# Kernel optimization log

Measured on AMD Instinct MI355X. Metric: run time of the kernel, lower is better.

Reference implementation:

```python
import jax, jax.numpy as jnp
import numpy as np

T, B, M = 2048, 256, 32


def setup_inputs() -> dict:
    key = jax.random.key(0)
    k1, k2, k3, k4 = jax.random.split(key, 4)
    emissions = jax.random.normal(k1, (T, B, M), jnp.float32)
    tags = jax.random.randint(k2, (T, B), 0, M)
    # weight divides transition scores -> keep strictly positive
    weight = jax.random.uniform(k3, (T, B), jnp.float32, 0.5, 1.5)
    mask = jnp.ones((T, B), jnp.int32)  # first timestep must be all-on
    transitions = jax.random.normal(k4, (M, M), jnp.float32) * 0.1
    start_transitions = jnp.zeros((M,), jnp.float32)
    end_transitions = jnp.zeros((M,), jnp.float32)
    return {
        "emissions": emissions,
        "tags": tags,
        "weight": weight,
        "mask": mask,
        "transitions": transitions,
        "start_transitions": start_transitions,
        "end_transitions": end_transitions,
    }


def reference(emissions, tags, weight, mask, transitions, start_transitions, end_transitions):
    # emissions: [T,B,M]; tags/weight/mask: [T,B]; reduction='sum' (torch default)
    Tn, Bn, Mn = emissions.shape
    maskb = mask.astype(bool)
    tags = jnp.where(maskb, tags, 1)
    maskf = mask.astype(emissions.dtype)

    # ---- gold-path score (_compute_score) ----
    score = start_transitions[tags[0]]
    score = score + (transitions[tags[:-1], tags[1:]] * maskf[1:] / weight[:-1]).sum(0)
    em_sc = jnp.take_along_axis(emissions, tags[:, :, None], axis=-1)[..., 0] * maskf
    score = score + em_sc.sum(0)
    seq_ends = mask.astype(jnp.int32).sum(0) - 1  # [B]
    last_tags = tags[seq_ends, jnp.arange(Bn)]
    score = score + end_transitions[last_tags]

    # ---- log-partition (_compute_normalizer) via logsumexp-semiring scan ----
    neg_inf = jnp.asarray(-jnp.inf, emissions.dtype)
    log_eye = jnp.where(jnp.eye(Mn, dtype=bool), jnp.zeros((), emissions.dtype), neg_inf)

    alpha0 = start_transitions + emissions[0]  # [B,M]

    def step(alpha, xs):
        em_t, w_t, m_t = xs  # [B,M], [B], [B]
        sc = transitions[None, :, :] / w_t[:, None, None] + em_t[:, None, :]  # [B,M,M]
        sc = jnp.where(m_t[:, None, None], sc, log_eye)  # masked step = identity in log-semiring
        alpha = jax.nn.logsumexp(alpha[:, :, None] + sc, axis=1)
        return alpha, None

    alpha, _ = jax.lax.scan(step, alpha0, (emissions[1:], weight[:-1], maskb[1:]))
    log_Z = jax.nn.logsumexp(alpha + end_transitions, axis=1)  # [B]

    nllh = log_Z - score
    return nllh.sum()
```

## Files before the change

kernel.cpp:

```cpp
#include <hip/hip_runtime.h>
#include <hip/hip_bf16.h>
#include <stdint.h>


#define T_DIM 2048
#define B_DIM 256
#define M_DIM 32
#define CHUNKS 32
#define CLEN 64
#define KSC 184.6649652337873f
#define SBIAS2 12599160.66f

typedef __attribute__((ext_vector_type(8))) short short8;
typedef __attribute__((ext_vector_type(16))) float f32x16;

__device__ __forceinline__ int pack_bf16(float lo, float hi) {
  union { float f; uint32_t u; } a, b;
  a.f = lo; b.f = hi;
  return (int)__builtin_amdgcn_perm(b.u, a.u, 0x07060302u);
}

__device__ __forceinline__ int pack_lo16(int lo, int hi) {
  return (int)__builtin_amdgcn_perm((uint32_t)hi, (uint32_t)lo, 0x05040100u);
}

__device__ __forceinline__ float bcast_lane(float v, int idx) {
  return __int_as_float(__builtin_amdgcn_readlane(__float_as_int(v), idx));
}

__global__ __launch_bounds__(256) void chunk_kernel(
    const float* __restrict__ em, const int* __restrict__ tags,
    const float* __restrict__ wt, const int* __restrict__ mask,
    const float* __restrict__ trans, const float* __restrict__ endt,
    uint32_t* __restrict__ mats, float* __restrict__ offs,
    float* __restrict__ out)
{
  int tid = threadIdx.x;
  int lane = tid & 63;
  int h = lane >> 5;
  int r = lane & 31;
  int wid = blockIdx.x * 4 + (tid >> 6);
  int u0 = 4 * wid;
  int bb = u0 & (B_DIM - 1);
  int c = u0 >> 8;
  int t0 = 1 + c * CLEN;
  int t1 = t0 + CLEN; if (t1 > T_DIM) t1 = T_DIM;

  float tpre[16];
#pragma unroll
  for (int j = 0; j < 8; ++j) {
    int row = ((j < 4) ? j : j + 4) + 4 * h;
    tpre[j]     = trans[row * 32 + r] * KSC;
    tpre[8 + j] = trans[(row + 16) * 32 + r] * KSC;
  }

  int tw = t0 - 1 + lane; if (tw > T_DIM - 1) tw = T_DIM - 1;
  int tmk = t0 + lane; if (tmk > T_DIM - 1) tmk = T_DIM - 1;
  float rwv[4];
  uint64_t mk[4];
  uint64_t valid = (t1 - t0 >= 64) ? ~0ull : ((1ull << (t1 - t0)) - 1ull);
#pragma unroll
  for (int ch = 0; ch < 4; ++ch) {
    rwv[ch] = __builtin_amdgcn_rcpf(wt[tw * B_DIM + bb + ch]);
    mk[ch] = __ballot(mask[tmk * B_DIM + bb + ch] != 0) & valid;
  }

  f32x16 X[4];
#pragma unroll
  for (int p = 0; p < 16; ++p) {
    float v = (((p & 3) + 8 * (p >> 2) + 4 * h) == r) ? 1.f : 0.f;
    X[0][p] = v; X[1][p] = v; X[2][p] = v; X[3][p] = v;
  }
  f32x16 z;
#pragma unroll
  for (int u = 0; u < 16; ++u) z[u] = 0.f;

  float off2[4] = {0.f, 0.f, 0.f, 0.f};

  auto step = [&](f32x16& Xc, float e_em, float rw) {
    float e = fmaf(e_em, KSC, SBIAS2);
    float qf[16];
#pragma unroll
    for (int j = 0; j < 16; ++j)
      qf[j] = fmaf(tpre[j], rw, e);
    union { int i[4]; short8 s; } af1, af2;
#pragma unroll
    for (int u = 0; u < 4; ++u) {
      af1.i[u] = pack_lo16(__float_as_int(qf[2 * u]),     __float_as_int(qf[2 * u + 1]));
      af2.i[u] = pack_lo16(__float_as_int(qf[8 + 2 * u]), __float_as_int(qf[8 + 2 * u + 1]));
    }
    union { int i[4]; short8 s; } b1_, b2_;
#pragma unroll
    for (int u = 0; u < 4; ++u) {
      b1_.i[u] = pack_bf16(Xc[2 * u],     Xc[2 * u + 1]);
      b2_.i[u] = pack_bf16(Xc[8 + 2 * u], Xc[8 + 2 * u + 1]);
    }
    f32x16 d = __builtin_amdgcn_mfma_f32_32x32x16_bf16(af1.s, b1_.s, z, 0, 0, 0);
    Xc = __builtin_amdgcn_mfma_f32_32x32x16_bf16(af2.s, b2_.s, d, 0, 0, 0);
  };

  auto rescale = [&](f32x16& Xc, float& o2) {
    float mx = Xc[0];
#pragma unroll
    for (int u = 1; u < 16; ++u) mx = fmaxf(mx, Xc[u]);
#pragma unroll
    for (int off = 1; off < 64; off <<= 1) mx = fmaxf(mx, __shfl_xor(mx, off));
    float sc = __builtin_amdgcn_rcpf(mx);
    o2 += __builtin_amdgcn_logf(mx);
#pragma unroll
    for (int u = 0; u < 16; ++u) Xc[u] *= sc;
  };

  bool fast = (t1 - t0 == 64) && (mk[0] == ~0ull) && (mk[1] == ~0ull)
            && (mk[2] == ~0ull) && (mk[3] == ~0ull);

  if (fast) {
    float e[4][4], n[4][4];
#pragma unroll
    for (int ch = 0; ch < 4; ++ch)
#pragma unroll
      for (int u = 0; u < 4; ++u)
        e[ch][u] = em[((size_t)((t0 + 2 * u + h) * B_DIM + bb + ch)) * 32 + r];
    for (int g = 0; g < 8; ++g) {
      int tg = t0 + 8 * (g + 1);
#pragma unroll
      for (int ch = 0; ch < 4; ++ch)
#pragma unroll
        for (int u = 0; u < 4; ++u) {
          int tt = tg + 2 * u + h; if (tt > T_DIM - 1) tt = T_DIM - 1;
          n[ch][u] = em[((size_t)(tt * B_DIM + bb + ch)) * 32 + r];
        }
#pragma unroll
      for (int u = 0; u < 4; ++u) {
        int sA = 8 * g + 2 * u, sB = sA + 1;
        float sw[4];
#pragma unroll
        for (int ch = 0; ch < 4; ++ch) sw[ch] = __shfl_xor(e[ch][u], 32);
#pragma unroll
        for (int ch = 0; ch < 4; ++ch)
          step(X[ch], h ? sw[ch] : e[ch][u], bcast_lane(rwv[ch], sA));
#pragma unroll
        for (int ch = 0; ch < 4; ++ch)
          step(X[ch], h ? e[ch][u] : sw[ch], bcast_lane(rwv[ch], sB));
      }
#pragma unroll
      for (int ch = 0; ch < 4; ++ch) rescale(X[ch], off2[ch]);
#pragma unroll
      for (int ch = 0; ch < 4; ++ch)
#pragma unroll
        for (int u = 0; u < 4; ++u) e[ch][u] = n[ch][u];
    }
  } else {
    float emv[4], emp[4];
#pragma unroll
    for (int ch = 0; ch < 4; ++ch)
      emv[ch] = em[((size_t)((t0 + h) * B_DIM + bb + ch)) * 32 + r];
    int tpf = t0 + 2 + h; if (tpf > T_DIM - 1) tpf = T_DIM - 1;
#pragma unroll
    for (int ch = 0; ch < 4; ++ch)
      emp[ch] = em[((size_t)(tpf * B_DIM + bb + ch)) * 32 + r];

    for (int it = 0; it < CLEN / 2; ++it) {
      int tn = t0 + 2 * it + 4 + h; if (tn > T_DIM - 1) tn = T_DIM - 1;
      float emn[4];
#pragma unroll
      for (int ch = 0; ch < 4; ++ch)
        emn[ch] = em[((size_t)(tn * B_DIM + bb + ch)) * 32 + r];

      int sA = 2 * it, sB = sA + 1;
#pragma unroll
      for (int ch = 0; ch < 4; ++ch) {
        float sw = __shfl_xor(emv[ch], 32);
        if ((mk[ch] >> sA) & 1)
          step(X[ch], h ? sw : emv[ch], bcast_lane(rwv[ch], sA));
        if ((t0 + sB < t1) && ((mk[ch] >> sB) & 1))
          step(X[ch], h ? emv[ch] : sw, bcast_lane(rwv[ch], sB));
      }

      if ((it & 3) == 3) {
#pragma unroll
        for (int ch = 0; ch < 4; ++ch) rescale(X[ch], off2[ch]);
      }
#pragma unroll
      for (int ch = 0; ch < 4; ++ch) { emv[ch] = emp[ch]; emp[ch] = emn[ch]; }
    }
  }

#pragma unroll
  for (int ch = 0; ch < 4; ++ch) {
    uint32_t* mp = mats + (size_t)(u0 + ch) * 512;
#pragma unroll
    for (int u = 0; u < 8; ++u) {
      int pairIdx = (u & 1) + (u >> 1) * 4 + 2 * h;
      mp[pairIdx * 32 + r] = (uint32_t)pack_bf16(X[ch][2 * u], X[ch][2 * u + 1]);
    }
  }
  if (lane == 0) {
#pragma unroll
    for (int ch = 0; ch < 4; ++ch) offs[u0 + ch] = off2[ch];
  }

  int t = t0 + lane;
  float ssc = 0.f;
  if (t < t1) {
#pragma unroll
    for (int ch = 0; ch < 4; ++ch) {
      int b = bb + ch;
      int mkc  = mask[t * B_DIM + b];
      int mkn  = (t + 1 < T_DIM) ? mask[(t + 1) * B_DIM + b] : 0;
      int tg   = mkc ? tags[t * B_DIM + b] : 1;
      int mkp  = mask[(t - 1) * B_DIM + b];
      int tgp  = mkp ? tags[(t - 1) * B_DIM + b] : 1;
      if (mkc)
        ssc += em[(size_t)(t * B_DIM + b) * 32 + tg]
             + trans[tgp * 32 + tg] * __builtin_amdgcn_rcpf(wt[(t - 1) * B_DIM + b]);
      if (mkc && !mkn) ssc += endt[tg];
    }
  }
#pragma unroll
  for (int off = 32; off; off >>= 1) ssc += __shfl_xor(ssc, off);
  if (lane == 0) atomicAdd(out, -ssc);
}

__global__ __launch_bounds__(64) void combine_kernel(
    const float* __restrict__ em, const int* __restrict__ tags,
    const int* __restrict__ mask, const float* __restrict__ startt,
    const float* __restrict__ endt, const uint32_t* __restrict__ mats,
    const float* __restrict__ offs, float* __restrict__ out)
{
  const float INV_LN2 = 1.44269504088896340736f;
  const float LN2 = 0.69314718055994530942f;
  int lane = threadIdx.x;
  int j = lane & 31;
  int h = lane >> 5;
  int b = blockIdx.x;
  int jp = j >> 1, jh = j & 1;

  float a0 = (startt[j] + em[(size_t)b * 32 + j]) * INV_LN2;
  float c0 = a0;
#pragma unroll
  for (int off = 1; off < 32; off <<= 1) c0 = fmaxf(c0, __shfl_xor(c0, off));
  float av = __builtin_amdgcn_exp2f(a0 - c0);
  float acc = c0;

  const uint4* xr0 = (const uint4*)(mats + (size_t)b * 512 + jp * 32 + 16 * h);
  uint4 nv0 = xr0[0], nv1 = xr0[1];
  float noff = offs[b];

  for (int c = 0; c < CHUNKS; ++c) {
    uint4 v0 = nv0, v1 = nv1;
    float offc = noff;
    int cn = (c + 1 < CHUNKS) ? c + 1 : c;
    const uint4* xrn = (const uint4*)(mats + (size_t)(cn * B_DIM + b) * 512 + jp * 32 + 16 * h);
    nv0 = xrn[0]; nv1 = xrn[1];
    noff = offs[cn * B_DIM + b];

    float x[8];
    uint32_t u0[4] = {v0.x, v0.y, v0.z, v0.w};
    uint32_t u1[4] = {v1.x, v1.y, v1.z, v1.w};
#pragma unroll
    for (int e = 0; e < 4; ++e) {
      uint32_t bits0 = jh ? (u0[e] & 0xFFFF0000u) : (u0[e] << 16);
      uint32_t bits1 = jh ? (u1[e] & 0xFFFF0000u) : (u1[e] << 16);
      union { uint32_t uu; float f; } cv0, cv1;
      cv0.uu = bits0; cv1.uu = bits1;
      x[e] = cv0.f; x[4 + e] = cv1.f;
    }
    float s0 = 0.f, s1 = 0.f;
#pragma unroll
    for (int i = 0; i < 4; ++i) {
      s0 = fmaf(x[i],     __shfl(av, 16 * h + i),     s0);
      s1 = fmaf(x[4 + i], __shfl(av, 16 * h + 4 + i), s1);
    }
    float an = s0 + s1;
    an += __shfl_xor(an, 32);
    float mx = an;
#pragma unroll
    for (int off = 1; off < 32; off <<= 1) mx = fmaxf(mx, __shfl_xor(mx, off));
    av = an * __builtin_amdgcn_rcpf(mx);
    acc += __builtin_amdgcn_logf(mx) + offc;
  }

  float sv = av * __builtin_amdgcn_exp2f(endt[j] * INV_LN2);
#pragma unroll
  for (int off = 1; off < 32; off <<= 1) sv += __shfl_xor(sv, off);
  if (lane == 0) {
    float logZ = (acc + __builtin_amdgcn_logf(sv)) * LN2;
    int mk0 = mask[b];
    int tg0 = mk0 ? tags[b] : 1;
    float s0 = startt[tg0] + (mk0 ? em[(size_t)b * 32 + tg0] : 0.f);
    int mk1 = mask[B_DIM + b];
    if (mk0 && !mk1) s0 += endt[tg0];
    atomicAdd(out, logZ - s0);
  }
}

extern "C" void kernel_launch(void* const* d_in, const int* in_sizes, int n_in,
                              void* d_out, int out_size, void* d_ws, size_t ws_size,
                              hipStream_t stream) {
  const float* em   = (const float*)d_in[0];
  const int*   tags = (const int*)d_in[1];
  const float* wt   = (const float*)d_in[2];
  const int*   mask = (const int*)d_in[3];
  const float* tr   = (const float*)d_in[4];
  const float* stt  = (const float*)d_in[5];
  const float* ent  = (const float*)d_in[6];
  float* out = (float*)d_out;

  float* offs = (float*)d_ws;
  uint32_t* mats = (uint32_t*)(offs + CHUNKS * B_DIM);

  hipMemsetAsync(out, 0, sizeof(float) * out_size, stream);
  chunk_kernel<<<(CHUNKS * B_DIM) / 16, 256, 0, stream>>>(em, tags, wt, mask, tr, ent, mats, offs, out);
  combine_kernel<<<B_DIM, 64, 0, stream>>>(em, tags, mask, stt, ent, mats, offs, out);
}
```

Baseline: 190.6 us.

## Batch four chain steps for MFMA interleaving and deepen combine-kernel prefetch

The fast path of the chunk kernel now builds the operands for all four independent chains before issuing their MFMAs back to back. This lets the matrix pipeline overlap the four dependent two-MFMA sequences instead of serialising each chain's pack-then-multiply. The launch bounds request two blocks per SM, which caps register use. The combine kernel now prefetches four chunks ahead instead of one, to hide global load latency. The cost is higher register pressure, with a risk of spills under the tighter occupancy bound, and the prefetch indexing relies on `c & 3` into a register array.

```diff
diff --git a/kernel.cpp b/kernel.cpp
--- a/kernel.cpp
+++ b/kernel.cpp
@@ -28,7 +28,7 @@
   return __int_as_float(__builtin_amdgcn_readlane(__float_as_int(v), idx));
 }
 
-__global__ __launch_bounds__(256) void chunk_kernel(
+__global__ __launch_bounds__(256, 2) void chunk_kernel(
     const float* __restrict__ em, const int* __restrict__ tags,
     const float* __restrict__ wt, const int* __restrict__ mask,
     const float* __restrict__ trans, const float* __restrict__ endt,
@@ -77,26 +77,56 @@
 
   float off2[4] = {0.f, 0.f, 0.f, 0.f};
 
-  auto step = [&](f32x16& Xc, float e_em, float rw) {
+  auto step4 = [&](const float* e4, int s) {
+    float rw0 = bcast_lane(rwv[0], s), rw1 = bcast_lane(rwv[1], s);
+    float rw2 = bcast_lane(rwv[2], s), rw3 = bcast_lane(rwv[3], s);
+    float rw[4] = {rw0, rw1, rw2, rw3};
+    union { int i[4]; short8 s8; } af1[4], af2[4], b1[4], b2[4];
+#pragma unroll
+    for (int ch = 0; ch < 4; ++ch) {
+      float e = fmaf(e4[ch], KSC, SBIAS2);
+      float qf[16];
+#pragma unroll
+      for (int j = 0; j < 16; ++j)
+        qf[j] = fmaf(tpre[j], rw[ch], e);
+#pragma unroll
+      for (int u = 0; u < 4; ++u) {
+        af1[ch].i[u] = pack_lo16(__float_as_int(qf[2 * u]),     __float_as_int(qf[2 * u + 1]));
+        af2[ch].i[u] = pack_lo16(__float_as_int(qf[8 + 2 * u]), __float_as_int(qf[8 + 2 * u + 1]));
+      }
+    }
+#pragma unroll
+    for (int ch = 0; ch < 4; ++ch)
+#pragma unroll
+      for (int u = 0; u < 4; ++u) {
+        b1[ch].i[u] = pack_bf16(X[ch][2 * u],     X[ch][2 * u + 1]);
+        b2[ch].i[u] = pack_bf16(X[ch][8 + 2 * u], X[ch][8 + 2 * u + 1]);
+      }
+    f32x16 d[4];
+#pragma unroll
+    for (int ch = 0; ch < 4; ++ch)
+      d[ch] = __builtin_amdgcn_mfma_f32_32x32x16_bf16(af1[ch].s8, b1[ch].s8, z, 0, 0, 0);
+#pragma unroll
+    for (int ch = 0; ch < 4; ++ch)
+      X[ch] = __builtin_amdgcn_mfma_f32_32x32x16_bf16(af2[ch].s8, b2[ch].s8, d[ch], 0, 0, 0);
+  };
+
+  auto stepOne = [&](f32x16& Xc, float e_em, float rw) {
     float e = fmaf(e_em, KSC, SBIAS2);
     float qf[16];
 #pragma unroll
     for (int j = 0; j < 16; ++j)
       qf[j] = fmaf(tpre[j], rw, e);
-    union { int i[4]; short8 s; } af1, af2;
+    union { int i[4]; short8 s8; } af1, af2, b1_, b2_;
 #pragma unroll
     for (int u = 0; u < 4; ++u) {
       af1.i[u] = pack_lo16(__float_as_int(qf[2 * u]),     __float_as_int(qf[2 * u + 1]));
       af2.i[u] = pack_lo16(__float_as_int(qf[8 + 2 * u]), __float_as_int(qf[8 + 2 * u + 1]));
-    }
-    union { int i[4]; short8 s; } b1_, b2_;
-#pragma unroll
-    for (int u = 0; u < 4; ++u) {
       b1_.i[u] = pack_bf16(Xc[2 * u],     Xc[2 * u + 1]);
       b2_.i[u] = pack_bf16(Xc[8 + 2 * u], Xc[8 + 2 * u + 1]);
     }
-    f32x16 d = __builtin_amdgcn_mfma_f32_32x32x16_bf16(af1.s, b1_.s, z, 0, 0, 0);
-    Xc = __builtin_amdgcn_mfma_f32_32x32x16_bf16(af2.s, b2_.s, d, 0, 0, 0);
+    f32x16 d = __builtin_amdgcn_mfma_f32_32x32x16_bf16(af1.s8, b1_.s8, z, 0, 0, 0);
+    Xc = __builtin_amdgcn_mfma_f32_32x32x16_bf16(af2.s8, b2_.s8, d, 0, 0, 0);
   };
 
   auto rescale = [&](f32x16& Xc, float& o2) {
@@ -133,15 +163,15 @@
 #pragma unroll
       for (int u = 0; u < 4; ++u) {
         int sA = 8 * g + 2 * u, sB = sA + 1;
-        float sw[4];
-#pragma unroll
-        for (int ch = 0; ch < 4; ++ch) sw[ch] = __shfl_xor(e[ch][u], 32);
-#pragma unroll
-        for (int ch = 0; ch < 4; ++ch)
-          step(X[ch], h ? sw[ch] : e[ch][u], bcast_lane(rwv[ch], sA));
-#pragma unroll
-        for (int ch = 0; ch < 4; ++ch)
-          step(X[ch], h ? e[ch][u] : sw[ch], bcast_lane(rwv[ch], sB));
+        float eA[4], eB[4];
+#pragma unroll
+        for (int ch = 0; ch < 4; ++ch) {
+          float sw = __shfl_xor(e[ch][u], 32);
+          eA[ch] = h ? sw : e[ch][u];
+          eB[ch] = h ? e[ch][u] : sw;
+        }
+        step4(eA, sA);
+        step4(eB, sB);
       }
 #pragma unroll
       for (int ch = 0; ch < 4; ++ch) rescale(X[ch], off2[ch]);
@@ -172,9 +202,9 @@
       for (int ch = 0; ch < 4; ++ch) {
         float sw = __shfl_xor(emv[ch], 32);
         if ((mk[ch] >> sA) & 1)
-          step(X[ch], h ? sw : emv[ch], bcast_lane(rwv[ch], sA));
+          stepOne(X[ch], h ? sw : emv[ch], bcast_lane(rwv[ch], sA));
         if ((t0 + sB < t1) && ((mk[ch] >> sB) & 1))
-          step(X[ch], h ? emv[ch] : sw, bcast_lane(rwv[ch], sB));
+          stepOne(X[ch], h ? emv[ch] : sw, bcast_lane(rwv[ch], sB));
       }
 
       if ((it & 3) == 3) {
@@ -243,17 +273,24 @@
   float av = __builtin_amdgcn_exp2f(a0 - c0);
   float acc = c0;
 
-  const uint4* xr0 = (const uint4*)(mats + (size_t)b * 512 + jp * 32 + 16 * h);
-  uint4 nv0 = xr0[0], nv1 = xr0[1];
-  float noff = offs[b];
+  uint4 pv0[4], pv1[4];
+  float poff[4];
+#pragma unroll
+  for (int k = 0; k < 4; ++k) {
+    int ck = (k < CHUNKS) ? k : CHUNKS - 1;
+    const uint4* xr = (const uint4*)(mats + (size_t)(ck * B_DIM + b) * 512 + jp * 32 + 16 * h);
+    pv0[k] = xr[0]; pv1[k] = xr[1];
+    poff[k] = offs[ck * B_DIM + b];
+  }
 
   for (int c = 0; c < CHUNKS; ++c) {
-    uint4 v0 = nv0, v1 = nv1;
-    float offc = noff;
-    int cn = (c + 1 < CHUNKS) ? c + 1 : c;
+    int slot = c & 3;
+    uint4 v0 = pv0[slot], v1 = pv1[slot];
+    float offc = poff[slot];
+    int cn = c + 4; if (cn > CHUNKS - 1) cn = CHUNKS - 1;
     const uint4* xrn = (const uint4*)(mats + (size_t)(cn * B_DIM + b) * 512 + jp * 32 + 16 * h);
-    nv0 = xrn[0]; nv1 = xrn[1];
-    noff = offs[cn * B_DIM + b];
+    pv0[slot] = xrn[0]; pv1[slot] = xrn[1];
+    poff[slot] = offs[cn * B_DIM + b];
 
     float x[8];
     uint32_t u0[4] = {v0.x, v0.y, v0.z, v0.w};
```

New measurement: 208.3 us. 9.3% more time.
